# Kernel optimization log

Measured on AMD Instinct MI355X. Metric: run time of the kernel, lower is better.

The kernel has to match this reference:

```python
import jax, jax.numpy as jnp
import numpy as np

D_MODEL = 192
D_INNER = 384          # expand(2) * d_model
HEADDIM = 12
NHEADS = 32            # d_inner // headdim
DSTATE = 16
NGROUPS = 1
CONV_DIM = D_INNER + 2 * NGROUPS * DSTATE          # 416
D_IN_PROJ = 2 * D_INNER + 2 * NGROUPS * DSTATE + NHEADS  # 832
LN_EPS = 1e-5


def silu(x):
    return x * jax.nn.sigmoid(x)


def depthwise_conv2d(x_nchw, w, b):
    # groups == channels depthwise conv, kernel 3, padding 1 (SAME)
    out = jax.lax.conv_general_dilated(
        x_nchw, w, window_strides=(1, 1), padding='SAME',
        feature_group_count=CONV_DIM,
        dimension_numbers=('NCHW', 'OIHW', 'NCHW'))
    return out + b[None, :, None, None]


def setup_inputs() -> dict:
    key = jax.random.key(0)
    ks = jax.random.split(key, 10)
    Bn, H, W = 4, 128, 128
    u = jax.random.normal(ks[0], (Bn, H, W, D_MODEL), jnp.float32)
    t = jax.random.normal(ks[1], (Bn, H, W, D_MODEL), jnp.float32)
    s_in = 1.0 / np.sqrt(D_MODEL)
    W_in = jax.random.normal(ks[2], (D_IN_PROJ, D_MODEL), jnp.float32) * s_in
    W_t_in = jax.random.normal(ks[3], (D_IN_PROJ, D_MODEL), jnp.float32) * s_in
    conv_w = jax.random.normal(ks[4], (CONV_DIM, 1, 3, 3), jnp.float32) * (1.0 / 3.0)
    conv_b = jnp.zeros((CONV_DIM,), jnp.float32)
    # dt_bias = inverse-softplus of dt sampled log-uniform in [dt_min, dt_max]
    dt0 = jnp.exp(jax.random.uniform(ks[5], (NHEADS,)) * (np.log(0.1) - np.log(0.001)) + np.log(0.001))
    dt_bias = dt0 + jnp.log(-jnp.expm1(-dt0))
    A_log = jnp.log(jax.random.uniform(ks[6], (NHEADS,), minval=1.0, maxval=16.0))
    D = jnp.ones((NHEADS,), jnp.float32)
    ln_gamma = jnp.ones((D_INNER,), jnp.float32)
    ln_beta = jnp.zeros((D_INNER,), jnp.float32)
    W_out = jax.random.normal(ks[7], (D_MODEL, D_INNER), jnp.float32) * (1.0 / np.sqrt(D_INNER))
    return dict(u=u, t=t, W_in=W_in, W_t_in=W_t_in, conv_w=conv_w, conv_b=conv_b,
                dt_bias=dt_bias, A_log=A_log, D=D, ln_gamma=ln_gamma, ln_beta=ln_beta,
                W_out=W_out)


def reference(u, t, W_in, W_t_in, conv_w, conv_b, dt_bias, A_log, D,
              ln_gamma, ln_beta, W_out):
    B0, H, W_, C0 = u.shape
    L = H * W_
    uu = u.reshape(B0, L, C0)
    tt = t.reshape(B0, L, C0)

    # in_proj on main branch: split into z, xBC, dt
    zxbcdt = uu @ W_in.T                                    # (B, L, 832)
    z = zxbcdt[..., :D_INNER]                               # (B, L, 384)
    xBC = zxbcdt[..., D_INNER:D_INNER + CONV_DIM]           # (B, L, 416)
    dt = zxbcdt[..., D_INNER + CONV_DIM:]                   # (B, L, 32)
    dt = jax.nn.softplus(dt + dt_bias)

    # t branch: only x1B1C1 part is ultimately used (C := C1)
    x1B1C1 = (tt @ W_t_in.T)[..., D_INNER:D_INNER + CONV_DIM]

    # depthwise 3x3 conv + silu on both branches
    xBC = xBC.reshape(B0, H, W_, CONV_DIM).transpose(0, 3, 1, 2)
    xBC = silu(depthwise_conv2d(xBC, conv_w, conv_b))
    xBC = xBC.transpose(0, 2, 3, 1).reshape(B0, L, CONV_DIM)

    x1B1C1 = x1B1C1.reshape(B0, H, W_, CONV_DIM).transpose(0, 3, 1, 2)
    x1B1C1 = silu(depthwise_conv2d(x1B1C1, conv_w, conv_b))
    x1B1C1 = x1B1C1.transpose(0, 2, 3, 1).reshape(B0, L, CONV_DIM)

    x = xBC[..., :D_INNER]                                  # V features (B, L, 384)
    Bk = xBC[..., D_INNER:D_INNER + NGROUPS * DSTATE]       # K (B, L, 16)
    Cq = x1B1C1[..., D_INNER + NGROUPS * DSTATE:]           # Q from t-branch (B, L, 16)

    A = -jnp.exp(A_log)                                     # (nheads,), negative

    # non-causal linear attention duality (ngroups == 1)
    V = x.reshape(B0, L, NHEADS, HEADDIM).transpose(0, 2, 1, 3)   # (B, h, L, d)
    dtT = dt.transpose(0, 2, 1)                                   # (B, h, L)
    dA = -(dtT[..., None] * A[None, :, None, None])               # ssd_positve_dA: positive
    V_scaled = V * dA
    KV = jnp.einsum('bln,bhld->bhnd', Bk, V_scaled)               # (B, h, 16, 12)
    y = jnp.einsum('bln,bhnd->bhld', Cq, KV) + V * D[None, :, None, None]
    y = y.transpose(0, 2, 1, 3).reshape(B0, L, D_INNER)

    # LayerNorm over d_inner
    mu = jnp.mean(y, axis=-1, keepdims=True)
    var = jnp.mean((y - mu) ** 2, axis=-1, keepdims=True)
    y = (y - mu) * jax.lax.rsqrt(var + LN_EPS) * ln_gamma + ln_beta

    y = y * z
    out = y @ W_out.T
    return out.reshape(B0, H, W_, C0)
```

## Files before the change

### kernel.cpp

```cpp
#include <hip/hip_runtime.h>
#include <hip/hip_bf16.h>
#include <math.h>


#define BN 4
#define HH 128
#define WWID 128
#define LTOK (HH*WWID)
#define NTOK (BN*LTOK)
#define DMODEL 192
#define DINNER 384
#define NH 32
#define HD 12
#define DST 16
#define CONVD 416
#define KVCHUNKS 64
#define PSTR 200

typedef __hip_bfloat16 bf16;
typedef unsigned int uint32;
typedef unsigned short ushort16;
typedef __attribute__((ext_vector_type(8))) short bf16x8;
typedef __attribute__((ext_vector_type(4))) float f32x4;

__device__ __forceinline__ float bflo(uint32 v){ return __uint_as_float((v & 0xffffu) << 16); }
__device__ __forceinline__ float bfhi(uint32 v){ return __uint_as_float(v & 0xffff0000u); }
__device__ __forceinline__ ushort16 f2bf(float f){
    __hip_bfloat16 h = __float2bfloat16(f);
    return *reinterpret_cast<const ushort16*>(&h);
}
__device__ __forceinline__ float softplusf(float x){
    return (x > 20.f) ? x : log1pf(expf(x));
}
__device__ __forceinline__ float siluf(float x){
    return x / (1.f + expf(-x));
}

union BFPK { short s[8]; bf16x8 v; };

__global__ __launch_bounds__(256) void k_prep(
    const float* __restrict__ Win, const float* __restrict__ Wout,
    const float* __restrict__ cw,
    bf16* __restrict__ Winbf, bf16* __restrict__ Woutbf, float* __restrict__ wtr)
{
    const int i = blockIdx.x*256 + threadIdx.x;
    if (i < 832*DMODEL)   Winbf[i]  = __float2bfloat16(Win[i]);
    if (i < DMODEL*DINNER) Woutbf[i] = __float2bfloat16(Wout[i]);
    if (i < CONVD*9) { const int c = i/9, k = i - c*9; wtr[k*420 + c] = cw[i]; }
}

__global__ __launch_bounds__(256) void k_proj_mfma(
    const float* __restrict__ u, const bf16* __restrict__ Wbf,
    const float* __restrict__ dt_b, const float* __restrict__ A_log,
    bf16* __restrict__ z_bf, bf16* __restrict__ xbc_pre, float* __restrict__ dA)
{
    __shared__ __align__(16) short S[128*PSTR];

    const int tid = threadIdx.x;
    const int m0 = blockIdx.x * 128;
    const int wid = tid >> 6, lane = tid & 63;
    const int fr = lane & 15, fq = lane >> 4;

    {
        const int row = tid >> 1, half = tid & 1;
        const float* src = u + (size_t)(m0 + row)*DMODEL + half*96;
        short* dst = &S[row*PSTR + half*96];
        #pragma unroll
        for (int i = 0; i < 12; ++i) {
            const float4 a0 = *(const float4*)(src + i*8);
            const float4 a1 = *(const float4*)(src + i*8 + 4);
            BFPK pk;
            pk.s[0]=(short)f2bf(a0.x); pk.s[1]=(short)f2bf(a0.y);
            pk.s[2]=(short)f2bf(a0.z); pk.s[3]=(short)f2bf(a0.w);
            pk.s[4]=(short)f2bf(a1.x); pk.s[5]=(short)f2bf(a1.y);
            pk.s[6]=(short)f2bf(a1.z); pk.s[7]=(short)f2bf(a1.w);
            *(bf16x8*)(dst + i*8) = pk.v;
        }
    }
    __syncthreads();

    bf16x8 a[2][6];
    #pragma unroll
    for (int mi=0;mi<2;++mi)
        #pragma unroll
        for (int ks=0;ks<6;++ks)
            a[mi][ks] = *(const bf16x8*)&S[(wid*32 + mi*16 + fr)*PSTR + ks*32 + fq*8];
    __syncthreads();

    for (int nt = 0; nt < 7; ++nt) {
        {
            const int row = tid >> 1, half = tid & 1;
            const int ch = nt*128 + row;
            if (ch < 832) {
                const short* g = (const short*)Wbf + (size_t)ch*DMODEL + half*96;
                short* d = &S[row*PSTR + half*96];
                #pragma unroll
                for (int i=0;i<6;++i) {
                    *(uint4*)(d + i*16)     = *(const uint4*)(g + i*16);
                    *(uint4*)(d + i*16 + 8) = *(const uint4*)(g + i*16 + 8);
                }
            }
        }
        __syncthreads();

        f32x4 acc[2][8];
        #pragma unroll
        for (int mi=0;mi<2;++mi)
            #pragma unroll
            for (int ni=0;ni<8;++ni) acc[mi][ni] = (f32x4){0.f,0.f,0.f,0.f};

        #pragma unroll
        for (int ks=0;ks<6;++ks) {
            bf16x8 b[8];
            #pragma unroll
            for (int ni=0;ni<8;++ni)
                b[ni] = *(const bf16x8*)&S[(ni*16 + fr)*PSTR + ks*32 + fq*8];
            #pragma unroll
            for (int mi=0;mi<2;++mi)
                #pragma unroll
                for (int ni=0;ni<8;++ni)
                    acc[mi][ni] = __builtin_amdgcn_mfma_f32_16x16x32_bf16(a[mi][ks], b[ni], acc[mi][ni], 0, 0, 0);
        }
        __syncthreads();

        #pragma unroll
        for (int ni=0;ni<8;++ni) {
            const int idx16 = nt*8 + ni;
            if (idx16 >= 52) continue;
            const int n = idx16*16 + fr;
            #pragma unroll
            for (int mi=0;mi<2;++mi) {
                #pragma unroll
                for (int j=0;j<4;++j) {
                    const int tok = m0 + wid*32 + mi*16 + fq*4 + j;
                    const float v = acc[mi][ni][j];
                    if (idx16 < 24) {
                        z_bf[(size_t)tok*DINNER + n] = __float2bfloat16(v);
                    } else if (idx16 < 50) {
                        xbc_pre[(size_t)tok*CONVD + (n - DINNER)] = __float2bfloat16(v);
                    } else {
                        const int hh = n - 800;
                        const float dt = softplusf(v + dt_b[hh]);
                        dA[(size_t)tok*NH + hh] = dt * expf(A_log[hh]);
                    }
                }
            }
        }
    }
}

__global__ __launch_bounds__(256) void k_tproj(
    const float* __restrict__ t, const float* __restrict__ Wtin, float* __restrict__ cq_pre)
{
    __shared__ float ts[16][196];
    __shared__ float ws[16][196];
    const int tid = threadIdx.x;
    const int tok0 = blockIdx.x * 16;
    #pragma unroll
    for (int i = 0; i < 3; ++i) {
        const int flat = tid + 256*i;
        const int row = flat / 48, c = (flat % 48)*4;
        *(float4*)&ts[row][c] = *(const float4*)(t    + (size_t)(tok0+row)*DMODEL + c);
        *(float4*)&ws[row][c] = *(const float4*)(Wtin + (size_t)(784+row)*DMODEL + c);
    }
    __syncthreads();
    const int tt = tid >> 4, n = tid & 15;
    float s0=0.f,s1=0.f,s2=0.f,s3=0.f;
    #pragma unroll 4
    for (int k = 0; k < DMODEL; k += 4) {
        s0 = fmaf(ts[tt][k+0], ws[n][k+0], s0);
        s1 = fmaf(ts[tt][k+1], ws[n][k+1], s1);
        s2 = fmaf(ts[tt][k+2], ws[n][k+2], s2);
        s3 = fmaf(ts[tt][k+3], ws[n][k+3], s3);
    }
    cq_pre[(size_t)(tok0+tt)*DST + n] = (s0+s1)+(s2+s3);
}

__global__ __launch_bounds__(416) void k_conv416(
    const bf16* __restrict__ in, const float* __restrict__ wtr, const float* __restrict__ cb,
    bf16* __restrict__ out)
{
    __shared__ float ws[9*420];
    __shared__ float bs[416];
    const int tid = threadIdx.x;
    for (int i = tid; i < 9*420; i += 416) ws[i] = wtr[i];
    if (tid < 416) bs[tid] = cb[tid];
    __syncthreads();

    const int pl  = tid / 52;
    const int grp = tid - pl*52;
    const int c0  = grp*8;
    const int pix = blockIdx.x*8 + pl;
    const int hw  = pix & (LTOK-1);
    const int h = hw >> 7, w = hw & 127;
    const int bb = pix >> 14;

    float acc[8];
    {
        const float4 b0 = *(const float4*)&bs[c0];
        const float4 b1 = *(const float4*)&bs[c0+4];
        acc[0]=b0.x; acc[1]=b0.y; acc[2]=b0.z; acc[3]=b0.w;
        acc[4]=b1.x; acc[5]=b1.y; acc[6]=b1.z; acc[7]=b1.w;
    }

    #pragma unroll
    for (int dh=-1; dh<=1; ++dh) {
        const int hh = h + dh;
        if ((unsigned)hh >= (unsigned)HH) continue;
        #pragma unroll
        for (int dw=-1; dw<=1; ++dw) {
            const int w2 = w + dw;
            if ((unsigned)w2 >= (unsigned)WWID) continue;
            const int wi = (dh+1)*3 + (dw+1);
            const size_t off = ((size_t)((bb<<14) + (hh<<7) + w2))*CONVD + c0;
            const uint4 v = *(const uint4*)((const ushort16*)in + off);
            const float4 w0 = *(const float4*)&ws[wi*420 + c0];
            const float4 w1 = *(const float4*)&ws[wi*420 + c0 + 4];
            acc[0] = fmaf(bflo(v.x), w0.x, acc[0]);
            acc[1] = fmaf(bfhi(v.x), w0.y, acc[1]);
            acc[2] = fmaf(bflo(v.y), w0.z, acc[2]);
            acc[3] = fmaf(bfhi(v.y), w0.w, acc[3]);
            acc[4] = fmaf(bflo(v.z), w1.x, acc[4]);
            acc[5] = fmaf(bfhi(v.z), w1.y, acc[5]);
            acc[6] = fmaf(bflo(v.w), w1.z, acc[6]);
            acc[7] = fmaf(bfhi(v.w), w1.w, acc[7]);
        }
    }

    uint4 o;
    o.x = ((uint32)f2bf(siluf(acc[1])) << 16) | (uint32)f2bf(siluf(acc[0]));
    o.y = ((uint32)f2bf(siluf(acc[3])) << 16) | (uint32)f2bf(siluf(acc[2]));
    o.z = ((uint32)f2bf(siluf(acc[5])) << 16) | (uint32)f2bf(siluf(acc[4]));
    o.w = ((uint32)f2bf(siluf(acc[7])) << 16) | (uint32)f2bf(siluf(acc[6]));
    *(uint4*)((ushort16*)out + (size_t)pix*CONVD + c0) = o;
}

__global__ __launch_bounds__(256) void k_conv16(
    const float* __restrict__ in, const float* __restrict__ cw, const float* __restrict__ cb,
    float* __restrict__ out)
{
    const int idx = blockIdx.x*256 + threadIdx.x;
    const int cc = idx & 15;
    const int pix = idx >> 4;
    const int hw = pix & (LTOK-1);
    const int h = hw >> 7, w = hw & 127;
    const int bb = pix >> 14;
    const int c = 400 + cc;

    float wg[9];
    #pragma unroll
    for (int k=0;k<9;++k) wg[k] = cw[c*9+k];
    float a = cb[c];
    #pragma unroll
    for (int dh=-1; dh<=1; ++dh) {
        const int hh = h + dh;
        if ((unsigned)hh >= (unsigned)HH) continue;
        #pragma unroll
        for (int dw=-1; dw<=1; ++dw) {
            const int w2 = w + dw;
            if ((unsigned)w2 >= (unsigned)WWID) continue;
            a = fmaf(in[((size_t)((bb<<14)+(hh<<7)+w2))*16 + cc], wg[(dh+1)*3 + (dw+1)], a);
        }
    }
    out[(size_t)pix*16 + cc] = siluf(a);
}

__global__ __launch_bounds__(512) void k_kv(
    const bf16* __restrict__ xbc_post, const float* __restrict__ dA,
    float* __restrict__ partial)
{
    __shared__ short vsb[16][408];
    __shared__ float das[16][32];
    const int tid = threadIdx.x;
    const int b = blockIdx.y;
    const int n = tid & 15;
    const int g = tid >> 4;

    float acc[12];
    #pragma unroll
    for (int j=0;j<12;++j) acc[j]=0.f;

    const int l0base = b*LTOK + blockIdx.x*256;

    for (int it = 0; it < 16; ++it) {
        const int l0 = l0base + it*16;
        for (int i = tid; i < 16*200; i += 512) {
            const int tok = i / 200;
            const int c2 = i - tok*200;
            const uint32 v = *(const uint32*)((const ushort16*)xbc_post
                                + (size_t)(l0+tok)*CONVD + c2*2);
            *(uint32*)&vsb[tok][c2*2] = v;
        }
        {
            const int tok = tid >> 5, h = tid & 31;
            das[tok][h] = dA[(size_t)(l0+tok)*NH + h];
        }
        __syncthreads();

        #pragma unroll
        for (int tok = 0; tok < 16; ++tok) {
            const uint32 bkraw = (uint32)(ushort16)vsb[tok][DINNER + n];
            const float s = __uint_as_float(bkraw << 16) * das[tok][g];
            const uint32* vp = (const uint32*)&vsb[tok][g*12];
            const uint32 w0 = vp[0], w1 = vp[1], w2 = vp[2];
            acc[0]  = fmaf(s, bflo(w0), acc[0]);
            acc[1]  = fmaf(s, bfhi(w0), acc[1]);
            acc[2]  = fmaf(s, bflo(w1), acc[2]);
            acc[3]  = fmaf(s, bfhi(w1), acc[3]);
            acc[4]  = fmaf(s, bflo(w2), acc[4]);
            acc[5]  = fmaf(s, bfhi(w2), acc[5]);
            const uint32* vq = (const uint32*)&vsb[tok][g*12 + 6];
            const uint32 w3 = vq[0], w4 = vq[1], w5 = vq[2];
            acc[6]  = fmaf(s, bflo(w3), acc[6]);
            acc[7]  = fmaf(s, bfhi(w3), acc[7]);
            acc[8]  = fmaf(s, bflo(w4), acc[8]);
            acc[9]  = fmaf(s, bfhi(w4), acc[9]);
            acc[10] = fmaf(s, bflo(w5), acc[10]);
            acc[11] = fmaf(s, bfhi(w5), acc[11]);
        }
        __syncthreads();
    }

    float* dst = partial + ((size_t)(b*KVCHUNKS + blockIdx.x))*6144 + (size_t)tid*12;
    #pragma unroll
    for (int j4=0;j4<3;++j4)
        *(float4*)(dst + j4*4) = make_float4(acc[j4*4], acc[j4*4+1], acc[j4*4+2], acc[j4*4+3]);
}

__global__ __launch_bounds__(256) void k_kvred(
    const float* __restrict__ partial, float* __restrict__ kv)
{
    const int idx = blockIdx.x*256 + threadIdx.x;
    const int b = idx / 6144;
    const int flat = idx - b*6144;
    const float* p = partial + (size_t)(b*KVCHUNKS)*6144 + flat;
    float s = 0.f;
    #pragma unroll 4
    for (int c = 0; c < KVCHUNKS; ++c) s += p[(size_t)c*6144];
    kv[idx] = s;
}

__global__ __launch_bounds__(256) void k_ynorm(
    const bf16* __restrict__ xbc_post, const float* __restrict__ cq_post,
    const bf16* __restrict__ z_bf, const float* __restrict__ kv,
    const float* __restrict__ Dv, const float* __restrict__ ln_g, const float* __restrict__ ln_b,
    bf16* __restrict__ yz)
{
    __shared__ float kvs[NH*DST*HD];
    __shared__ float ys[16][386];
    __shared__ float cqs[16][16];
    const int tid = threadIdx.x;
    const int token0 = blockIdx.x * 16;
    const int b = token0 >> 14;

    for (int i = tid; i < NH*DST*HD; i += 256) {
        const int n = i / DINNER;
        const int hd = i - n*DINNER;
        const int h = hd / HD;
        const int d = hd - h*HD;
        kvs[i] = kv[((size_t)(b*NH + h)*DST + n)*HD + d];
    }
    {
        const int tt = tid >> 4, n2 = tid & 15;
        cqs[tt][n2] = cq_post[(size_t)(token0+tt)*DST + n2];
    }
    __syncthreads();

    #pragma unroll
    for (int jj=0; jj<12; ++jj) {
        const int flat = jj*256 + tid;
        const int tt = flat / 192;
        const int p  = flat - tt*192;
        const int hd = p*2;
        const int h = hd / HD;
        const int l = token0 + tt;
        const uint32 v = *(const uint32*)((const ushort16*)xbc_post + (size_t)l*CONVD + hd);
        const float dv = Dv[h];
        float a0 = bflo(v) * dv;
        float a1 = bfhi(v) * dv;
        #pragma unroll
        for (int n=0;n<16;++n) {
            const float c = cqs[tt][n];
            const float2 kk = *(const float2*)&kvs[n*DINNER + hd];
            a0 = fmaf(c, kk.x, a0);
            a1 = fmaf(c, kk.y, a1);
        }
        *(float2*)&ys[tt][hd] = make_float2(a0, a1);
    }
    __syncthreads();

    const int wave = tid >> 6, lane = tid & 63;
    #pragma unroll
    for (int i=0;i<4;++i) {
        const int tt = wave*4 + i;
        const int l = token0 + tt;
        float v[6]; float s=0.f, s2=0.f;
        #pragma unroll
        for (int k=0;k<6;++k){ const float x = ys[tt][k*64+lane]; v[k]=x; s+=x; s2=fmaf(x,x,s2); }
        #pragma unroll
        for (int off=32; off>0; off>>=1){ s += __shfl_xor(s,off,64); s2 += __shfl_xor(s2,off,64); }
        const float mu = s*(1.f/384.f);
        const float var = s2*(1.f/384.f) - mu*mu;
        const float rs = rsqrtf(var + 1e-5f);
        #pragma unroll
        for (int k=0;k<6;++k){
            const int idx = k*64+lane;
            const float yn = (v[k]-mu)*rs*ln_g[idx] + ln_b[idx];
            const uint32 zb = (uint32)(*((const ushort16*)z_bf + (size_t)l*DINNER + idx));
            const float zv = __uint_as_float(zb << 16);
            yz[(size_t)l*DINNER + idx] = __float2bfloat16(yn*zv);
        }
    }
}

__global__ __launch_bounds__(256) void k_out_mfma(
    const bf16* __restrict__ yz, const bf16* __restrict__ Wbf, float* __restrict__ out)
{
    __shared__ __align__(16) short As[2][128*40];
    __shared__ __align__(16) short Bs[2][192*40];

    const int tid = threadIdx.x;
    const int m0 = blockIdx.x * 128;
    const int wid = tid >> 6, lane = tid & 63;
    const int wm = wid >> 1, wn = wid & 1;
    const int fr = lane & 15, fq = lane >> 4;

    const int arow = tid >> 1, ahalf = tid & 1;
    auto stageA = [&](int ks, int buf) {
        const short* g = (const short*)yz + (size_t)(m0 + arow)*DINNER + ks*32 + ahalf*16;
        const uint4 v0 = *(const uint4*)g;
        const uint4 v1 = *(const uint4*)(g + 8);
        short* d = &As[buf][arow*40 + ahalf*16];
        *(uint4*)d = v0;
        *(uint4*)(d + 8) = v1;
    };
    auto stageB = [&](int ks, int buf) {
        #pragma unroll
        for (int i = 0; i < 3; ++i) {
            const int flat = tid + 256*i;
            const int row = flat >> 2, q = flat & 3;
            const uint4 v = *(const uint4*)((const short*)Wbf + (size_t)row*DINNER + ks*32 + q*8);
            *(uint4*)&Bs[buf][row*40 + q*8] = v;
        }
    };

    f32x4 acc[4][6];
    #pragma unroll
    for (int mi=0;mi<4;++mi)
        #pragma unroll
        for (int ni=0;ni<6;++ni) acc[mi][ni] = (f32x4){0.f,0.f,0.f,0.f};

    stageA(0, 0); stageB(0, 0);
    __syncthreads();

    const int aoff = (wm*64 + fr)*40 + fq*8;
    const int boff = (wn*96 + fr)*40 + fq*8;

    #pragma unroll
    for (int ks = 0; ks < 12; ++ks) {
        const int cur = ks & 1;
        if (ks < 11) { stageA(ks+1, cur^1); stageB(ks+1, cur^1); }
        bf16x8 a[4], b[6];
        #pragma unroll
        for (int mi=0;mi<4;++mi) a[mi] = *(const bf16x8*)(&As[cur][aoff + mi*640]);
        #pragma unroll
        for (int ni=0;ni<6;++ni) b[ni] = *(const bf16x8*)(&Bs[cur][boff + ni*640]);
        #pragma unroll
        for (int mi=0;mi<4;++mi)
            #pragma unroll
            for (int ni=0;ni<6;++ni)
                acc[mi][ni] = __builtin_amdgcn_mfma_f32_16x16x32_bf16(a[mi], b[ni], acc[mi][ni], 0, 0, 0);
        __syncthreads();
    }

    #pragma unroll
    for (int mi=0;mi<4;++mi) {
        #pragma unroll
        for (int j=0;j<4;++j) {
            const int tok = m0 + wm*64 + mi*16 + fq*4 + j;
            #pragma unroll
            for (int ni=0;ni<6;++ni) {
                const int n = wn*96 + ni*16 + fr;
                out[(size_t)tok*DMODEL + n] = acc[mi][ni][j];
            }
        }
    }
}

extern "C" void kernel_launch(void* const* d_in, const int* in_sizes, int n_in,
                              void* d_out, int out_size, void* d_ws, size_t ws_size,
                              hipStream_t stream)
{
    const float* u      = (const float*)d_in[0];
    const float* t      = (const float*)d_in[1];
    const float* Win    = (const float*)d_in[2];
    const float* Wtin   = (const float*)d_in[3];
    const float* conv_w = (const float*)d_in[4];
    const float* conv_b = (const float*)d_in[5];
    const float* dt_b   = (const float*)d_in[6];
    const float* A_log  = (const float*)d_in[7];
    const float* Dv     = (const float*)d_in[8];
    const float* ln_g   = (const float*)d_in[9];
    const float* ln_bt  = (const float*)d_in[10];
    const float* W_out  = (const float*)d_in[11];
    float* out = (float*)d_out;

    char* p = (char*)d_ws;
    bf16* z_bf     = (bf16*)p;  p += (size_t)NTOK*DINNER*2;
    bf16* xbc_pre  = (bf16*)p;  p += (size_t)NTOK*CONVD*2;
    bf16* xbc_post = (bf16*)p;  p += (size_t)NTOK*CONVD*2;
    float* cq_pre  = (float*)p; p += (size_t)NTOK*DST*4;
    float* cq_post = (float*)p; p += (size_t)NTOK*DST*4;
    float* dA      = (float*)p; p += (size_t)NTOK*NH*4;
    bf16* yz       = (bf16*)p;  p += (size_t)NTOK*DINNER*2;
    float* kv      = (float*)p; p += (size_t)BN*NH*DST*HD*4;
    bf16* Win_bf   = (bf16*)p;  p += (size_t)832*DMODEL*2;
    bf16* Wout_bf  = (bf16*)p;  p += (size_t)DMODEL*DINNER*2;
    float* wtr     = (float*)p; p += (size_t)9*420*4;

    float* kv_part = (float*)xbc_pre;

    k_prep<<<624, 256, 0, stream>>>(Win, W_out, conv_w, Win_bf, Wout_bf, wtr);
    k_proj_mfma<<<512, 256, 0, stream>>>(u, Win_bf, dt_b, A_log, z_bf, xbc_pre, dA);
    k_tproj<<<NTOK/16, 256, 0, stream>>>(t, Wtin, cq_pre);
    k_conv416<<<NTOK/8, 416, 0, stream>>>(xbc_pre, wtr, conv_b, xbc_post);
    k_conv16<<<NTOK*16/256, 256, 0, stream>>>(cq_pre, conv_w, conv_b, cq_post);
    k_kv<<<dim3(KVCHUNKS, BN), 512, 0, stream>>>(xbc_post, dA, kv_part);
    k_kvred<<<BN*6144/256, 256, 0, stream>>>(kv_part, kv);
    k_ynorm<<<NTOK/16, 256, 0, stream>>>(xbc_post, cq_post, z_bf, kv,
                                         Dv, ln_g, ln_bt, yz);
    k_out_mfma<<<512, 256, 0, stream>>>(yz, Wout_bf, out);
}
```

Before: 318.1 us.

## Restructure input projection GEMM with 32x32 MFMA and double-buffered weight tiles

Rewrites the input-projection kernel to use 256-token blocks with 512 threads, loading A fragments directly from global memory into registers instead of staging them through shared memory. Weight tiles of 64 channels are double-buffered in LDS, with register prefetch of the next tile overlapping the current MFMA work. The 16x16x32 MFMAs are replaced with 32x32x16 ones. The intent is to cut LDS traffic and barriers and hide weight-load latency, at the cost of fewer blocks (256) and more per-thread registers.

```diff
diff --git a/kernel.cpp b/kernel.cpp
--- a/kernel.cpp
+++ b/kernel.cpp
@@ -15,13 +15,16 @@
 #define DST 16
 #define CONVD 416
 #define KVCHUNKS 64
-#define PSTR 200
+#define PM 256
+#define PBN 64
+#define BSTR 200
 
 typedef __hip_bfloat16 bf16;
 typedef unsigned int uint32;
 typedef unsigned short ushort16;
 typedef __attribute__((ext_vector_type(8))) short bf16x8;
 typedef __attribute__((ext_vector_type(4))) float f32x4;
+typedef __attribute__((ext_vector_type(16))) float f32x16;
 
 __device__ __forceinline__ float bflo(uint32 v){ return __uint_as_float((v & 0xffffu) << 16); }
 __device__ __forceinline__ float bfhi(uint32 v){ return __uint_as_float(v & 0xffff0000u); }
@@ -49,103 +52,105 @@
     if (i < CONVD*9) { const int c = i/9, k = i - c*9; wtr[k*420 + c] = cw[i]; }
 }
 
-__global__ __launch_bounds__(256) void k_proj_mfma(
+__global__ __launch_bounds__(512) void k_proj_mfma(
     const float* __restrict__ u, const bf16* __restrict__ Wbf,
     const float* __restrict__ dt_b, const float* __restrict__ A_log,
     bf16* __restrict__ z_bf, bf16* __restrict__ xbc_pre, float* __restrict__ dA)
 {
-    __shared__ __align__(16) short S[128*PSTR];
+    __shared__ __align__(16) short S[2][PBN*BSTR];
 
     const int tid = threadIdx.x;
-    const int m0 = blockIdx.x * 128;
+    const int m0 = blockIdx.x * PM;
     const int wid = tid >> 6, lane = tid & 63;
-    const int fr = lane & 15, fq = lane >> 4;
-
+    const int fr = lane & 31;
+    const int hi = lane >> 5;
+
+    bf16x8 a[12];
     {
-        const int row = tid >> 1, half = tid & 1;
-        const float* src = u + (size_t)(m0 + row)*DMODEL + half*96;
-        short* dst = &S[row*PSTR + half*96];
-        #pragma unroll
-        for (int i = 0; i < 12; ++i) {
-            const float4 a0 = *(const float4*)(src + i*8);
-            const float4 a1 = *(const float4*)(src + i*8 + 4);
+        const float* arow = u + (size_t)(m0 + wid*32 + fr)*DMODEL;
+        #pragma unroll
+        for (int ks=0;ks<12;++ks) {
+            const float4 a0 = *(const float4*)(arow + ks*16 + hi*8);
+            const float4 a1 = *(const float4*)(arow + ks*16 + hi*8 + 4);
             BFPK pk;
             pk.s[0]=(short)f2bf(a0.x); pk.s[1]=(short)f2bf(a0.y);
             pk.s[2]=(short)f2bf(a0.z); pk.s[3]=(short)f2bf(a0.w);
             pk.s[4]=(short)f2bf(a1.x); pk.s[5]=(short)f2bf(a1.y);
             pk.s[6]=(short)f2bf(a1.z); pk.s[7]=(short)f2bf(a1.w);
-            *(bf16x8*)(dst + i*8) = pk.v;
-        }
-    }
+            a[ks] = pk.v;
+        }
+    }
+
+    const int srow = tid >> 3;
+    const int sseg = tid & 7;
+    uint4 r0, r1, r2;
+    auto LOADB = [&](int nt) {
+        const short* g = (const short*)Wbf + (size_t)(nt*PBN + srow)*DMODEL + sseg*24;
+        r0 = *(const uint4*)g;
+        r1 = *(const uint4*)(g + 8);
+        r2 = *(const uint4*)(g + 16);
+    };
+    auto WRITEB = [&](int buf) {
+        short* d = &S[buf][srow*BSTR + sseg*24];
+        *(uint4*)d        = r0;
+        *(uint4*)(d + 8)  = r1;
+        *(uint4*)(d + 16) = r2;
+    };
+
+    LOADB(0); WRITEB(0);
+    LOADB(1);
     __syncthreads();
 
-    bf16x8 a[2][6];
-    #pragma unroll
-    for (int mi=0;mi<2;++mi)
-        #pragma unroll
-        for (int ks=0;ks<6;++ks)
-            a[mi][ks] = *(const bf16x8*)&S[(wid*32 + mi*16 + fr)*PSTR + ks*32 + fq*8];
-    __syncthreads();
-
-    for (int nt = 0; nt < 7; ++nt) {
-        {
-            const int row = tid >> 1, half = tid & 1;
-            const int ch = nt*128 + row;
-            if (ch < 832) {
-                const short* g = (const short*)Wbf + (size_t)ch*DMODEL + half*96;
-                short* d = &S[row*PSTR + half*96];
+    for (int nt = 0; nt < 13; ++nt) {
+        const int cur = nt & 1;
+
+        f32x16 acc0, acc1;
+        #pragma unroll
+        for (int i=0;i<16;++i) { acc0[i]=0.f; acc1[i]=0.f; }
+
+        const short* Sb = &S[cur][0];
+        #pragma unroll
+        for (int ks=0;ks<12;++ks) {
+            const bf16x8 b0 = *(const bf16x8*)&Sb[(fr     )*BSTR + ks*16 + hi*8];
+            const bf16x8 b1 = *(const bf16x8*)&Sb[(32 + fr)*BSTR + ks*16 + hi*8];
+            acc0 = __builtin_amdgcn_mfma_f32_32x32x16_bf16(a[ks], b0, acc0, 0, 0, 0);
+            acc1 = __builtin_amdgcn_mfma_f32_32x32x16_bf16(a[ks], b1, acc1, 0, 0, 0);
+        }
+
+        #pragma unroll
+        for (int ni=0;ni<2;++ni) {
+            const f32x16& ac = ni ? acc1 : acc0;
+            const int n0 = nt*64 + ni*32;
+            const int n  = n0 + fr;
+            if (n0 < DINNER) {
                 #pragma unroll
-                for (int i=0;i<6;++i) {
-                    *(uint4*)(d + i*16)     = *(const uint4*)(g + i*16);
-                    *(uint4*)(d + i*16 + 8) = *(const uint4*)(g + i*16 + 8);
+                for (int r=0;r<16;++r) {
+                    const int tok = m0 + wid*32 + (r&3) + 8*(r>>2) + 4*hi;
+                    z_bf[(size_t)tok*DINNER + n] = __float2bfloat16(ac[r]);
+                }
+            } else if (n0 < 800) {
+                #pragma unroll
+                for (int r=0;r<16;++r) {
+                    const int tok = m0 + wid*32 + (r&3) + 8*(r>>2) + 4*hi;
+                    xbc_pre[(size_t)tok*CONVD + (n - DINNER)] = __float2bfloat16(ac[r]);
+                }
+            } else {
+                const float db = dt_b[fr];
+                const float al = expf(A_log[fr]);
+                #pragma unroll
+                for (int r=0;r<16;++r) {
+                    const int tok = m0 + wid*32 + (r&3) + 8*(r>>2) + 4*hi;
+                    const float dt = softplusf(ac[r] + db);
+                    dA[(size_t)tok*NH + fr] = dt * al;
                 }
             }
         }
+
+        if (nt < 12) {
+            WRITEB(cur ^ 1);
+            if (nt < 11) LOADB(nt + 2);
+        }
         __syncthreads();
-
-        f32x4 acc[2][8];
-        #pragma unroll
-        for (int mi=0;mi<2;++mi)
-            #pragma unroll
-            for (int ni=0;ni<8;++ni) acc[mi][ni] = (f32x4){0.f,0.f,0.f,0.f};
-
-        #pragma unroll
-        for (int ks=0;ks<6;++ks) {
-            bf16x8 b[8];
-            #pragma unroll
-            for (int ni=0;ni<8;++ni)
-                b[ni] = *(const bf16x8*)&S[(ni*16 + fr)*PSTR + ks*32 + fq*8];
-            #pragma unroll
-            for (int mi=0;mi<2;++mi)
-                #pragma unroll
-                for (int ni=0;ni<8;++ni)
-                    acc[mi][ni] = __builtin_amdgcn_mfma_f32_16x16x32_bf16(a[mi][ks], b[ni], acc[mi][ni], 0, 0, 0);
-        }
-        __syncthreads();
-
-        #pragma unroll
-        for (int ni=0;ni<8;++ni) {
-            const int idx16 = nt*8 + ni;
-            if (idx16 >= 52) continue;
-            const int n = idx16*16 + fr;
-            #pragma unroll
-            for (int mi=0;mi<2;++mi) {
-                #pragma unroll
-                for (int j=0;j<4;++j) {
-                    const int tok = m0 + wid*32 + mi*16 + fq*4 + j;
-                    const float v = acc[mi][ni][j];
-                    if (idx16 < 24) {
-                        z_bf[(size_t)tok*DINNER + n] = __float2bfloat16(v);
-                    } else if (idx16 < 50) {
-                        xbc_pre[(size_t)tok*CONVD + (n - DINNER)] = __float2bfloat16(v);
-                    } else {
-                        const int hh = n - 800;
-                        const float dt = softplusf(v + dt_b[hh]);
-                        dA[(size_t)tok*NH + hh] = dt * expf(A_log[hh]);
-                    }
-                }
-            }
-        }
     }
 }
 
@@ -521,7 +526,7 @@
     float* kv_part = (float*)xbc_pre;
 
     k_prep<<<624, 256, 0, stream>>>(Win, W_out, conv_w, Win_bf, Wout_bf, wtr);
-    k_proj_mfma<<<512, 256, 0, stream>>>(u, Win_bf, dt_b, A_log, z_bf, xbc_pre, dA);
+    k_proj_mfma<<<NTOK/PM, 512, 0, stream>>>(u, Win_bf, dt_b, A_log, z_bf, xbc_pre, dA);
     k_tproj<<<NTOK/16, 256, 0, stream>>>(t, Wtin, cq_pre);
     k_conv416<<<NTOK/8, 416, 0, stream>>>(xbc_pre, wtr, conv_b, xbc_post);
     k_conv16<<<NTOK*16/256, 256, 0, stream>>>(cq_pre, conv_w, conv_b, cq_post);
```

Measured after the change: 313.4 us. No clear change (-1.5%).
